# Optimization experiments

Measured on AMD Instinct MI355X. Metric: run time of the kernel, lower is better.

The kernel has to match this reference:

```python
import jax, jax.numpy as jnp
import numpy as np
import math

# Layer config: stride-8 feature map of a 608x608 YOLOv4 (anchor indices 6..8)
ANCHORS = np.array([[142,110],[192,243],[459,401],
                    [36,75],[76,55],[72,146],
                    [12,16],[19,36],[40,28]], dtype=np.float32)
NUM_CLASSES = 80
STRIDE = 8.0
ANCHOR_OFFSET = 6   # anchor_index [6,7,8], subtract_index 6 for in_w = 608//8 = 76
IGNORE_THRESH = 0.5
LABEL_SMOOTH = 0.0


def bce(pred, target):
    eps = 1e-7
    p = jnp.clip(pred, eps, 1.0 - eps)
    return -target * jnp.log(p) - (1.0 - target) * jnp.log(1.0 - p)


def box_ciou(b1, b2):
    # b1, b2: (..., 4) xywh in feature-map units
    b1_xy, b1_wh = b1[..., :2], b1[..., 2:4]
    b2_xy, b2_wh = b2[..., :2], b2[..., 2:4]
    b1_min, b1_max = b1_xy - b1_wh / 2.0, b1_xy + b1_wh / 2.0
    b2_min, b2_max = b2_xy - b2_wh / 2.0, b2_xy + b2_wh / 2.0
    iwh = jnp.maximum(jnp.minimum(b1_max, b2_max) - jnp.maximum(b1_min, b2_min), 0.0)
    inter = iwh[..., 0] * iwh[..., 1]
    union = b1_wh[..., 0] * b1_wh[..., 1] + b2_wh[..., 0] * b2_wh[..., 1] - inter
    iou = inter / jnp.maximum(union, 1e-6)
    center_d = jnp.sum((b1_xy - b2_xy) ** 2, axis=-1)
    ewh = jnp.maximum(jnp.maximum(b1_max, b2_max) - jnp.minimum(b1_min, b2_min), 0.0)
    enclose_diag = jnp.sum(ewh ** 2, axis=-1)
    ciou = iou - center_d / jnp.maximum(enclose_diag, 1e-6)
    v = (4.0 / math.pi ** 2) * (jnp.arctan(b1_wh[..., 0] / jnp.maximum(b1_wh[..., 1], 1e-6))
                                - jnp.arctan(b2_wh[..., 0] / jnp.maximum(b2_wh[..., 1], 1e-6))) ** 2
    alpha = v / jnp.maximum(1.0 - iou + v, 1e-6)
    return ciou - alpha * v


def yolo_loss(input, targets_boxes, targets_cls):
    bs, _, in_h, in_w = input.shape
    A, C = 3, NUM_CLASSES
    sa = jnp.asarray(ANCHORS) / STRIDE                       # (9,2) scaled anchors
    pred = input.reshape(bs, A, 5 + C, in_h, in_w).transpose(0, 1, 3, 4, 2)  # (bs,3,H,W,5+C)
    conf = jax.nn.sigmoid(pred[..., 4])
    pred_cls = jax.nn.sigmoid(pred[..., 5:])

    # ---------- get_target: best-anchor assignment + scatter into grid ----------
    T = targets_boxes.shape[1]
    gx = targets_boxes[..., 0] * in_w
    gy = targets_boxes[..., 1] * in_h
    gw = targets_boxes[..., 2] * in_w
    gh = targets_boxes[..., 3] * in_h
    aw, ah = sa[:, 0], sa[:, 1]
    # IoU of origin-centered boxes: inter = min(w)*min(h)
    inter_a = jnp.minimum(gw[..., None], aw) * jnp.minimum(gh[..., None], ah)
    union_a = gw[..., None] * gh[..., None] + aw * ah - inter_a
    best_n = jnp.argmax(inter_a / union_a, axis=-1)          # (bs,T)
    gi = jnp.floor(gx).astype(jnp.int32)
    gj = jnp.floor(gy).astype(jnp.int32)
    valid = (best_n >= ANCHOR_OFFSET) & (best_n < ANCHOR_OFFSET + A) & (gi < in_w) & (gj < in_h)
    a = jnp.clip(best_n - ANCHOR_OFFSET, 0, A - 1)
    N = bs * A * in_h * in_w
    b_idx = jnp.broadcast_to(jnp.arange(bs)[:, None], (bs, T))
    lin = ((b_idx * A + a) * in_h + gj) * in_w + gi
    lin = jnp.where(valid, lin, N).reshape(-1)               # invalid targets -> dummy slot N

    def scat(vals):
        buf = jnp.zeros(N + 1, jnp.float32).at[lin].set(vals.reshape(-1).astype(jnp.float32))
        return buf[:N].reshape(bs, A, in_h, in_w)

    mask = scat(jnp.ones((bs, T), jnp.float32))
    noobj_mask = 1.0 - mask
    t_box = jnp.stack([scat(gx), scat(gy), scat(gw), scat(gh)], axis=-1)  # (bs,3,H,W,4)
    box_loss_scale_x = scat(targets_boxes[..., 2])
    box_loss_scale_y = scat(targets_boxes[..., 3])
    cls_idx = lin * C + targets_cls.reshape(-1).astype(jnp.int32)
    tcls = jnp.zeros((N + 1) * C, jnp.float32).at[cls_idx].set(1.0)[:N * C]
    tcls = tcls.reshape(bs, A, in_h, in_w, C)

    # ---------- get_ignore: decode pred boxes, suppress high-IoU noobj ----------
    layer_anchors = sa[ANCHOR_OFFSET:ANCHOR_OFFSET + A]      # (3,2)
    grid_x = jnp.arange(in_w, dtype=jnp.float32)
    grid_y = jnp.arange(in_h, dtype=jnp.float32)[:, None]
    px = jax.nn.sigmoid(pred[..., 0]) + grid_x
    py = jax.nn.sigmoid(pred[..., 1]) + grid_y
    pw = jnp.exp(pred[..., 2]) * layer_anchors[:, 0][None, :, None, None]
    ph = jnp.exp(pred[..., 3]) * layer_anchors[:, 1][None, :, None, None]
    pred_boxes = jnp.stack([px, py, pw, ph], axis=-1)        # (bs,3,H,W,4)

    gt = jnp.stack([gx, gy, gw, gh], axis=-1)                # (bs,T,4)
    pb = pred_boxes.reshape(bs, -1, 4)                       # (bs,M,4), M = 3*H*W
    g1, g2 = gt[..., :2] - gt[..., 2:] / 2.0, gt[..., :2] + gt[..., 2:] / 2.0
    p1, p2 = pb[..., :2] - pb[..., 2:] / 2.0, pb[..., :2] + pb[..., 2:] / 2.0
    iwh = jnp.maximum(jnp.minimum(g2[:, :, None], p2[:, None]) - jnp.maximum(g1[:, :, None], p1[:, None]), 0.0)
    inter = iwh[..., 0] * iwh[..., 1]                        # (bs,T,M)
    area_g = (gt[..., 2] * gt[..., 3])[:, :, None]
    area_p = (pb[..., 2] * pb[..., 3])[:, None, :]
    iou = inter / (area_g + area_p - inter)
    iou_max = jnp.max(iou, axis=1).reshape(bs, A, in_h, in_w)
    noobj_mask = jnp.where(iou_max > IGNORE_THRESH, 0.0, noobj_mask)

    # ---------- losses ----------
    box_loss_scale = 2.0 - box_loss_scale_x * box_loss_scale_y
    ciou_term = (1.0 - box_ciou(pred_boxes, t_box)) * box_loss_scale
    loss_loc = jnp.sum(mask * ciou_term) / bs
    bce_conf = bce(conf, mask)
    loss_conf = jnp.sum(bce_conf * mask) / bs + jnp.sum(bce_conf * noobj_mask) / bs
    tcls_s = tcls * (1.0 - LABEL_SMOOTH) + LABEL_SMOOTH / C
    loss_cls = jnp.sum(mask[..., None] * bce(pred_cls, tcls_s)) / bs
    loss = loss_conf + loss_cls + loss_loc
    return loss, loss_conf, loss_cls, loss_loc


def setup_inputs() -> dict:
    key = jax.random.key(0)
    k1, k2, k3 = jax.random.split(key, 3)
    bs, T, H, W = 8, 50, 76, 76
    inp = jax.random.normal(k1, (bs, 3 * (5 + NUM_CLASSES), H, W), dtype=jnp.float32)
    tb = jax.random.uniform(k2, (bs, T, 4), dtype=jnp.float32)   # normalized xywh in [0,1)
    tc = jax.random.randint(k3, (bs, T), 0, NUM_CLASSES, dtype=jnp.int32)
    return {"input": inp, "targets_boxes": tb, "targets_cls": tc}


def reference(input, targets_boxes, targets_cls):
    return yolo_loss(input, targets_boxes, targets_cls)
```

## Files before the change

### kernel.cpp

```cpp
#include <hip/hip_runtime.h>
#include <math.h>

#define HH 76
#define WW 76
#define HW (HH*WW)
#define AA 3
#define CC 80
#define TT 50
#define BS 8
#define NPB (AA*HW)
#define CHUNKS ((NPB + 255) / 256)
#define NBLK (CHUNKS*BS)

__constant__ float c_aw[9] = {17.75f, 24.0f, 57.375f, 4.5f, 9.5f, 9.0f, 1.5f, 2.375f, 5.0f};
__constant__ float c_ah[9] = {13.75f, 30.375f, 50.125f, 9.375f, 6.875f, 18.25f, 2.0f, 4.5f, 3.5f};

__device__ __forceinline__ float sigf(float x) { return 1.0f / (1.0f + expf(-x)); }

__global__ __launch_bounds__(256) void yolo_main(const float* __restrict__ in,
                                                 const float* __restrict__ tb,
                                                 const int* __restrict__ tc,
                                                 float* __restrict__ part)
{
    __shared__ float4 sA[TT];
    __shared__ float4 sB[TT];
    __shared__ float4 sC[TT];
    __shared__ float  sred[3][4];

    const int b = blockIdx.y;
    const int tid = threadIdx.x;

    if (tid < TT) {
        int t = b * TT + tid;
        float t0 = tb[t*4 + 0];
        float t1 = tb[t*4 + 1];
        float t2 = tb[t*4 + 2];
        float t3 = tb[t*4 + 3];
        float gx = t0 * (float)WW;
        float gy = t1 * (float)HH;
        float gw = t2 * (float)WW;
        float gh = t3 * (float)HH;

        int best = 0;
        float bestv = -1.0f;
        float ag = gw * gh;
        #pragma unroll
        for (int n = 0; n < 9; n++) {
            float inter = fminf(gw, c_aw[n]) * fminf(gh, c_ah[n]);
            float uni   = ag + c_aw[n]*c_ah[n] - inter;
            float r = inter / uni;
            if (r > bestv) { bestv = r; best = n; }
        }
        int gi = (int)floorf(gx);
        int gj = (int)floorf(gy);
        bool valid = (best >= 6) && (best < 9) && (gi < WW) && (gj < HH);
        int a = best - 6; a = a < 0 ? 0 : (a > 2 ? 2 : a);
        int lin = valid ? ((a*HH + gj)*WW + gi) : -1;

        sA[tid] = make_float4(gx - 0.5f*gw, gy - 0.5f*gh, gx + 0.5f*gw, gy + 0.5f*gh);
        sB[tid] = make_float4(ag, 2.0f - t2*t3, __int_as_float(lin), __int_as_float(tc[t]));
        sC[tid] = make_float4(gx, gy, gw, gh);
    }
    __syncthreads();

    float accConf = 0.0f, accCls = 0.0f, accLoc = 0.0f;
    const int n = blockIdx.x * 256 + tid;
    if (n < NPB) {
        const int hw = n % HW;
        const int i  = n % WW;
        const int j  = (n / WW) % HH;
        const int a  = n / HW;

        const float* p = in + ((size_t)b*(AA*(5+CC)) + (size_t)a*(5+CC))*HW + hw;
        float tx  = p[0];
        float ty  = p[HW];
        float tw  = p[2*HW];
        float th  = p[3*HW];
        float tcf = p[4*HW];

        float px = sigf(tx) + (float)i;
        float py = sigf(ty) + (float)j;
        float pw = expf(tw) * c_aw[6 + a];
        float ph = expf(th) * c_ah[6 + a];
        float conf = sigf(tcf);

        float p1x = px - 0.5f*pw, p2x = px + 0.5f*pw;
        float p1y = py - 0.5f*ph, p2y = py + 0.5f*ph;
        float areap = pw * ph;

        float ioumax = 0.0f;
        int match = -1;
        #pragma unroll 10
        for (int t = 0; t < TT; t++) {
            float4 A = sA[t];
            float4 B = sB[t];
            float iw = fmaxf(fminf(A.z, p2x) - fmaxf(A.x, p1x), 0.0f);
            float ih = fmaxf(fminf(A.w, p2y) - fmaxf(A.y, p1y), 0.0f);
            float inter = iw * ih;
            float iou = inter * __builtin_amdgcn_rcpf(B.x + areap - inter);
            ioumax = fmaxf(ioumax, iou);
            if (__float_as_int(B.z) == n) match = t;
        }

        float pcl = fminf(fmaxf(conf, 1e-7f), 1.0f - 1e-7f);
        if (match >= 0) {
            accConf = -logf(pcl);
        } else if (ioumax <= 0.5f) {
            accConf = -logf(1.0f - pcl);
        }

        if (match >= 0) {
            float4 G = sC[match];
            float gx = G.x, gy = G.y, gw = G.z, gh = G.w;
            float bls = sB[match].y;
            float g1x = gx - 0.5f*gw, g2x = gx + 0.5f*gw;
            float g1y = gy - 0.5f*gh, g2y = gy + 0.5f*gh;
            float iw = fmaxf(fminf(p2x, g2x) - fmaxf(p1x, g1x), 0.0f);
            float ih = fmaxf(fminf(p2y, g2y) - fmaxf(p1y, g1y), 0.0f);
            float inter = iw * ih;
            float uni = areap + gw*gh - inter;
            float iou = inter / fmaxf(uni, 1e-6f);
            float dx = px - gx, dy = py - gy;
            float cd = dx*dx + dy*dy;
            float ewx = fmaxf(fmaxf(p2x, g2x) - fminf(p1x, g1x), 0.0f);
            float ewy = fmaxf(fmaxf(p2y, g2y) - fminf(p1y, g1y), 0.0f);
            float ediag = ewx*ewx + ewy*ewy;
            float ciou = iou - cd / fmaxf(ediag, 1e-6f);
            float da = atanf(pw / fmaxf(ph, 1e-6f)) - atanf(gw / fmaxf(gh, 1e-6f));
            const float PI2INV4 = 4.0f / (float)(M_PI * M_PI);
            float v = PI2INV4 * da * da;
            float alpha = v / fmaxf(1.0f - iou + v, 1e-6f);
            ciou = ciou - alpha * v;
            accLoc = (1.0f - ciou) * bls;

            unsigned b0 = 0, b1 = 0, b2 = 0;
            for (int t = 0; t < TT; t++) {
                if (__float_as_int(sB[t].z) == n) {
                    int c = __float_as_int(sB[t].w);
                    if (c < 32) b0 |= 1u << c;
                    else if (c < 64) b1 |= 1u << (c - 32);
                    else b2 |= 1u << (c - 64);
                }
            }
            const float* pc = p + 5*HW;
            #pragma unroll 8
            for (int c = 0; c < CC; c++) {
                float lg = pc[c*HW];
                float pp = fminf(fmaxf(sigf(lg), 1e-7f), 1.0f - 1e-7f);
                unsigned bit = (c < 32 ? (b0 >> c) : (c < 64 ? (b1 >> (c-32)) : (b2 >> (c-64)))) & 1u;
                float tgt = bit ? 1.0f : 0.0f;
                accCls += -(tgt * logf(pp) + (1.0f - tgt) * logf(1.0f - pp));
            }
        }
    }

    for (int off = 32; off > 0; off >>= 1) {
        accConf += __shfl_down(accConf, off);
        accCls  += __shfl_down(accCls,  off);
        accLoc  += __shfl_down(accLoc,  off);
    }
    int wid = tid >> 6;
    int lane = tid & 63;
    if (lane == 0) { sred[0][wid] = accConf; sred[1][wid] = accCls; sred[2][wid] = accLoc; }
    __syncthreads();
    if (tid == 0) {
        float c0 = 0.f, c1 = 0.f, c2 = 0.f;
        #pragma unroll
        for (int w = 0; w < 4; w++) { c0 += sred[0][w]; c1 += sred[1][w]; c2 += sred[2][w]; }
        const int bid = blockIdx.y * CHUNKS + blockIdx.x;
        part[0*NBLK + bid] = c0;
        part[1*NBLK + bid] = c1;
        part[2*NBLK + bid] = c2;
    }
}

__global__ __launch_bounds__(256) void yolo_fin(const float* __restrict__ part,
                                                float* __restrict__ out)
{
    __shared__ float sred[3][4];
    float c0 = 0.f, c1 = 0.f, c2 = 0.f;
    for (int k = threadIdx.x; k < NBLK; k += 256) {
        c0 += part[0*NBLK + k];
        c1 += part[1*NBLK + k];
        c2 += part[2*NBLK + k];
    }
    for (int off = 32; off > 0; off >>= 1) {
        c0 += __shfl_down(c0, off);
        c1 += __shfl_down(c1, off);
        c2 += __shfl_down(c2, off);
    }
    int wid = threadIdx.x >> 6;
    int lane = threadIdx.x & 63;
    if (lane == 0) { sred[0][wid] = c0; sred[1][wid] = c1; sred[2][wid] = c2; }
    __syncthreads();
    if (threadIdx.x == 0) {
        float s0 = 0.f, s1 = 0.f, s2 = 0.f;
        #pragma unroll
        for (int w = 0; w < 4; w++) { s0 += sred[0][w]; s1 += sred[1][w]; s2 += sred[2][w]; }
        const float inv_bs = 1.0f / (float)BS;
        s0 *= inv_bs; s1 *= inv_bs; s2 *= inv_bs;
        out[0] = s0 + s1 + s2;
        out[1] = s0;
        out[2] = s1;
        out[3] = s2;
    }
}

extern "C" void kernel_launch(void* const* d_in, const int* in_sizes, int n_in,
                              void* d_out, int out_size, void* d_ws, size_t ws_size,
                              hipStream_t stream) {
    const float* inp = (const float*)d_in[0];
    const float* tb  = (const float*)d_in[1];
    const int*   tc  = (const int*)d_in[2];
    float* out = (float*)d_out;
    float* part = (float*)d_ws;

    yolo_main<<<dim3(CHUNKS, BS), 256, 0, stream>>>(inp, tb, tc, part);
    yolo_fin<<<1, 256, 0, stream>>>(part, out);
}
```

Before: 108.6 us.

## Queue matched cells and compute class BCE cooperatively across a wavefront

Matched grid cells are no longer evaluated by one thread looping over all 80 class logits. Each one is pushed into a shared-memory queue together with its class bitmask. After a barrier, each wavefront takes queued cells and computes the 80 class terms in parallel, one class per lane, then reduces them with shuffles and a shared atomic. This removes the serial, divergent per-thread class loop and its strided loads. In exchange it adds an extra barrier, shared atomics, and some shared-memory repacking.

```diff
diff --git a/kernel.cpp b/kernel.cpp
--- a/kernel.cpp
+++ b/kernel.cpp
@@ -23,12 +23,19 @@
                                                  float* __restrict__ part)
 {
     __shared__ float4 sA[TT];
-    __shared__ float4 sB[TT];
+    __shared__ float2 sAL[TT];
     __shared__ float4 sC[TT];
-    __shared__ float  sred[3][4];
+    __shared__ float  sBls[TT];
+    __shared__ int    sCl[TT];
+    __shared__ int4   q[256];
+    __shared__ int    qcnt;
+    __shared__ float  sCls;
+    __shared__ float  sred[2][4];
 
     const int b = blockIdx.y;
     const int tid = threadIdx.x;
+
+    if (tid == 0) { qcnt = 0; sCls = 0.0f; }
 
     if (tid < TT) {
         int t = b * TT + tid;
@@ -57,13 +64,15 @@
         int a = best - 6; a = a < 0 ? 0 : (a > 2 ? 2 : a);
         int lin = valid ? ((a*HH + gj)*WW + gi) : -1;
 
-        sA[tid] = make_float4(gx - 0.5f*gw, gy - 0.5f*gh, gx + 0.5f*gw, gy + 0.5f*gh);
-        sB[tid] = make_float4(ag, 2.0f - t2*t3, __int_as_float(lin), __int_as_float(tc[t]));
-        sC[tid] = make_float4(gx, gy, gw, gh);
-    }
-    __syncthreads();
-
-    float accConf = 0.0f, accCls = 0.0f, accLoc = 0.0f;
+        sA[tid]   = make_float4(gx - 0.5f*gw, gy - 0.5f*gh, gx + 0.5f*gw, gy + 0.5f*gh);
+        sAL[tid]  = make_float2(ag, __int_as_float(lin));
+        sC[tid]   = make_float4(gx, gy, gw, gh);
+        sBls[tid] = 2.0f - t2*t3;
+        sCl[tid]  = tc[t];
+    }
+    __syncthreads();
+
+    float accConf = 0.0f, accLoc = 0.0f;
     const int n = blockIdx.x * 256 + tid;
     if (n < NPB) {
         const int hw = n % HW;
@@ -93,13 +102,13 @@
         #pragma unroll 10
         for (int t = 0; t < TT; t++) {
             float4 A = sA[t];
-            float4 B = sB[t];
+            float2 L = sAL[t];
             float iw = fmaxf(fminf(A.z, p2x) - fmaxf(A.x, p1x), 0.0f);
             float ih = fmaxf(fminf(A.w, p2y) - fmaxf(A.y, p1y), 0.0f);
             float inter = iw * ih;
-            float iou = inter * __builtin_amdgcn_rcpf(B.x + areap - inter);
+            float iou = inter * __builtin_amdgcn_rcpf(L.x + areap - inter);
             ioumax = fmaxf(ioumax, iou);
-            if (__float_as_int(B.z) == n) match = t;
+            if (__float_as_int(L.y) == n) match = t;
         }
 
         float pcl = fminf(fmaxf(conf, 1e-7f), 1.0f - 1e-7f);
@@ -112,7 +121,7 @@
         if (match >= 0) {
             float4 G = sC[match];
             float gx = G.x, gy = G.y, gw = G.z, gh = G.w;
-            float bls = sB[match].y;
+            float bls = sBls[match];
             float g1x = gx - 0.5f*gw, g2x = gx + 0.5f*gw;
             float g1y = gy - 0.5f*gh, g2y = gy + 0.5f*gh;
             float iw = fmaxf(fminf(p2x, g2x) - fmaxf(p1x, g1x), 0.0f);
@@ -135,41 +144,64 @@
 
             unsigned b0 = 0, b1 = 0, b2 = 0;
             for (int t = 0; t < TT; t++) {
-                if (__float_as_int(sB[t].z) == n) {
-                    int c = __float_as_int(sB[t].w);
+                if (__float_as_int(sAL[t].y) == n) {
+                    int c = sCl[t];
                     if (c < 32) b0 |= 1u << c;
                     else if (c < 64) b1 |= 1u << (c - 32);
                     else b2 |= 1u << (c - 64);
                 }
             }
-            const float* pc = p + 5*HW;
-            #pragma unroll 8
-            for (int c = 0; c < CC; c++) {
-                float lg = pc[c*HW];
-                float pp = fminf(fmaxf(sigf(lg), 1e-7f), 1.0f - 1e-7f);
-                unsigned bit = (c < 32 ? (b0 >> c) : (c < 64 ? (b1 >> (c-32)) : (b2 >> (c-64)))) & 1u;
-                float tgt = bit ? 1.0f : 0.0f;
-                accCls += -(tgt * logf(pp) + (1.0f - tgt) * logf(1.0f - pp));
-            }
-        }
+            int slot = atomicAdd(&qcnt, 1);
+            q[slot] = make_int4(n, (int)b0, (int)b1, (int)b2);
+        }
+    }
+    __syncthreads();
+
+    const int wid = tid >> 6;
+    const int lane = tid & 63;
+    const int cnt = qcnt;
+    for (int e = wid; e < cnt; e += 4) {
+        int4 Q = q[e];
+        int qn = Q.x;
+        int hw = qn % HW;
+        int a  = qn / HW;
+        const float* pc = in + ((size_t)b*(AA*(5+CC)) + (size_t)a*(5+CC) + 5)*HW + hw;
+        unsigned bits0 = (unsigned)Q.y, bits1 = (unsigned)Q.z, bits2 = (unsigned)Q.w;
+
+        int c0i = lane;
+        float lg0 = pc[(size_t)c0i * HW];
+        float v0;
+        {
+            float pp = fminf(fmaxf(sigf(lg0), 1e-7f), 1.0f - 1e-7f);
+            unsigned bit = (c0i < 32 ? (bits0 >> c0i) : (bits1 >> (c0i - 32))) & 1u;
+            v0 = bit ? -logf(pp) : -logf(1.0f - pp);
+        }
+        float v1 = 0.0f;
+        if (lane < CC - 64) {
+            int c1i = lane + 64;
+            float lg1 = pc[(size_t)c1i * HW];
+            float pp = fminf(fmaxf(sigf(lg1), 1e-7f), 1.0f - 1e-7f);
+            unsigned bit = (bits2 >> (c1i - 64)) & 1u;
+            v1 = bit ? -logf(pp) : -logf(1.0f - pp);
+        }
+        float s = v0 + v1;
+        for (int off = 32; off > 0; off >>= 1) s += __shfl_down(s, off);
+        if (lane == 0) atomicAdd(&sCls, s);
     }
 
     for (int off = 32; off > 0; off >>= 1) {
         accConf += __shfl_down(accConf, off);
-        accCls  += __shfl_down(accCls,  off);
         accLoc  += __shfl_down(accLoc,  off);
     }
-    int wid = tid >> 6;
-    int lane = tid & 63;
-    if (lane == 0) { sred[0][wid] = accConf; sred[1][wid] = accCls; sred[2][wid] = accLoc; }
+    if (lane == 0) { sred[0][wid] = accConf; sred[1][wid] = accLoc; }
     __syncthreads();
     if (tid == 0) {
-        float c0 = 0.f, c1 = 0.f, c2 = 0.f;
+        float c0 = 0.f, c2 = 0.f;
         #pragma unroll
-        for (int w = 0; w < 4; w++) { c0 += sred[0][w]; c1 += sred[1][w]; c2 += sred[2][w]; }
+        for (int w = 0; w < 4; w++) { c0 += sred[0][w]; c2 += sred[1][w]; }
         const int bid = blockIdx.y * CHUNKS + blockIdx.x;
         part[0*NBLK + bid] = c0;
-        part[1*NBLK + bid] = c1;
+        part[1*NBLK + bid] = sCls;
         part[2*NBLK + bid] = c2;
     }
 }
```

Measured after the change: 92.63 us. -14.7%, faster.
